# Kernel tuning notes

Hardware: AMD Instinct MI355X
Metric: run time of the kernel (lower is better)

## Reference

```python
import jax, jax.numpy as jnp
import numpy as np
import math

B, S, E, H = 2, 2048, 1024, 16
D = E // H  # head dim = 64


def setup_inputs() -> dict:
    key = jax.random.key(0)
    ks = jax.random.split(key, 7)
    scale = 1.0 / math.sqrt(E)
    return {
        "query": jax.random.normal(ks[0], (B, S, E), dtype=jnp.float32),
        "key": jax.random.normal(ks[1], (B, S, E), dtype=jnp.float32),
        "value": jax.random.normal(ks[2], (B, S, E), dtype=jnp.float32),
        # packed in-projection: (3E, E) weights, (3E,) bias, q/k/v order
        "in_proj_weight": jax.random.normal(ks[3], (3 * E, E), dtype=jnp.float32) * scale,
        "in_proj_bias": jnp.zeros((3 * E,), dtype=jnp.float32),
        "out_proj_weight": jax.random.normal(ks[4], (E, E), dtype=jnp.float32) * scale,
        "out_proj_bias": jnp.zeros((E,), dtype=jnp.float32),
    }


def reference(query, key, value, in_proj_weight, in_proj_bias, out_proj_weight, out_proj_bias):
    # packed in-projection (q, k, v order), F.linear convention: x @ W^T + b
    w_q, w_k, w_v = jnp.split(in_proj_weight, 3, axis=0)
    b_q, b_k, b_v = jnp.split(in_proj_bias, 3, axis=0)
    q = query @ w_q.T + b_q   # [B, S, E]
    k = key @ w_k.T + b_k
    v = value @ w_v.T + b_v

    # split heads: [B, S, E] -> [B, H, S, D]
    def heads(x):
        return x.reshape(B, S, H, D).transpose(0, 2, 1, 3)

    q, k, v = heads(q), heads(k), heads(v)
    q = q / jnp.asarray(math.sqrt(D), dtype=q.dtype)

    # naive softmax attention (materializes [B, H, S, S] as original bmm+softmax+bmm)
    scores = jnp.einsum("bhqd,bhkd->bhqk", q, k)
    attn = jax.nn.softmax(scores, axis=-1)
    out = jnp.einsum("bhqk,bhkd->bhqd", attn, v)  # [B, H, S, D]

    out = out.transpose(0, 2, 1, 3).reshape(B, S, E)
    return out @ out_proj_weight.T + out_proj_bias
```

## Files before the change

### kernel.cpp

```cpp
#include <hip/hip_runtime.h>
#include <stdint.h>

#define LOG2E 1.44269504088896340736f

typedef __bf16 bf16x8 __attribute__((ext_vector_type(8)));
typedef float f32x4 __attribute__((ext_vector_type(4)));
typedef float f32x16 __attribute__((ext_vector_type(16)));

static constexpr int Bb = 2, Ss = 2048, Ee = 1024, Hh = 16, Dd = 64;
static constexpr int BSE = Bb * Ss * Ee;

static constexpr size_t OFF_QB    = 0;
static constexpr size_t OFF_KB    = 4194304;
static constexpr size_t OFF_VB    = 8388608;
static constexpr size_t OFF_WQKV  = 12582912;
static constexpr size_t OFF_WOUT  = 15728640;
static constexpr size_t OFF_QH    = 16777216;
static constexpr size_t OFF_KH    = 20971520;
static constexpr size_t OFF_VH    = 25165824;
static constexpr size_t OFF_OB    = 29360128;

__device__ __forceinline__ uint16_t f32_bf16(float f) {
    uint32_t u = __builtin_bit_cast(uint32_t, f);
    u += 0x7fffu + ((u >> 16) & 1u);
    return (uint16_t)(u >> 16);
}

__device__ __forceinline__ uint32_t cvt_pk_bf16(float a, float b) {
    uint32_t r;
    asm("v_cvt_pk_bf16_f32 %0, %1, %2" : "=v"(r) : "v"(a), "v"(b));
    return r;
}

__device__ __forceinline__ void perm32swap(uint32_t& x, uint32_t& y) {
    asm("v_permlane32_swap_b32 %0, %1" : "+v"(x), "+v"(y));
}

__global__ __launch_bounds__(256) void cvt_kernel(
    const float* __restrict__ q, const float* __restrict__ k, const float* __restrict__ v,
    const float* __restrict__ w1, uint16_t* __restrict__ ws)
{
    const float* srcs[4] = {q, k, v, w1};
    const int ns4[4] = {BSE/4, BSE/4, BSE/4, (3*Ee*Ee)/4};
    uint16_t* dsts[4] = {ws+OFF_QB, ws+OFF_KB, ws+OFF_VB, ws+OFF_WQKV};
    int z = blockIdx.z;
    int i = blockIdx.x * blockDim.x + threadIdx.x;
    if (i < ns4[z]) {
        float4 f = ((const float4*)srcs[z])[i];
        ushort4 o;
        o.x = f32_bf16(f.x); o.y = f32_bf16(f.y);
        o.z = f32_bf16(f.z); o.w = f32_bf16(f.w);
        ((ushort4*)dsts[z])[i] = o;
    }
}

__global__ __launch_bounds__(256) void cvt_one(
    const float* __restrict__ src, uint16_t* __restrict__ dst)
{
    int i = blockIdx.x * 256 + threadIdx.x;
    float4 f = ((const float4*)src)[i];
    ushort4 o;
    o.x = f32_bf16(f.x); o.y = f32_bf16(f.y);
    o.z = f32_bf16(f.z); o.w = f32_bf16(f.w);
    ((ushort4*)dst)[i] = o;
}

template<int MODE>
__global__ __launch_bounds__(256) void gemm_nt(
    const uint16_t* __restrict__ Aq, const uint16_t* __restrict__ Ak,
    const uint16_t* __restrict__ Av, const uint16_t* __restrict__ Bw,
    const float* __restrict__ bias, uint16_t* __restrict__ OutB,
    float* __restrict__ OutF)
{
    constexpr int K = Ee, N = Ee;
    const int tid = threadIdx.x;
    const int l = tid & 63, w = tid >> 6;
    const int wr = w >> 1, wc = w & 1;
    const int z = (MODE == 0) ? blockIdx.z : 0;
    const int tm = 4 * blockIdx.x + (blockIdx.y >> 3);
    const int tn = blockIdx.y & 7;

    const uint16_t* A = (MODE == 0) ? (z == 0 ? Aq : (z == 1 ? Ak : Av)) : Aq;
    const uint16_t* Bp = Bw + (size_t)z * Ee * Ee;
    const float* bp = bias + (size_t)z * Ee;
    const size_t zoff = (size_t)(z == 2 ? 3 : z) * BSE;

    __shared__ alignas(16) uint16_t As[128 * 32];
    __shared__ alignas(16) uint16_t Bs[128 * 32];

    f32x4 acc[4][4] = {};
    const int arow = tm * 128;
    const int bcol = tn * 128;

    for (int kt = 0; kt < K / 32; ++kt) {
        __syncthreads();
        #pragma unroll
        for (int it = 0; it < 2; ++it) {
            int c = tid + it * 256;
            int row = c >> 2, qq = c & 3;
            const uint16_t* ga = A  + (size_t)(arow + row) * K + kt * 32 + qq * 8;
            const uint16_t* gb = Bp + (size_t)(bcol + row) * K + kt * 32 + qq * 8;
            __builtin_amdgcn_global_load_lds(
                (const __attribute__((address_space(1))) void*)ga,
                (__attribute__((address_space(3))) void*)(As + c * 8), 16, 0, 0);
            __builtin_amdgcn_global_load_lds(
                (const __attribute__((address_space(1))) void*)gb,
                (__attribute__((address_space(3))) void*)(Bs + c * 8), 16, 0, 0);
        }
        __syncthreads();
        bf16x8 aF[4], bF[4];
        #pragma unroll
        for (int m = 0; m < 4; ++m)
            aF[m] = *(const bf16x8*)(As + ((wr * 64 + m * 16 + (l & 15)) * 32 + (l >> 4) * 8));
        #pragma unroll
        for (int n = 0; n < 4; ++n)
            bF[n] = *(const bf16x8*)(Bs + ((wc * 64 + n * 16 + (l & 15)) * 32 + (l >> 4) * 8));
        #pragma unroll
        for (int m = 0; m < 4; ++m)
            #pragma unroll
            for (int n = 0; n < 4; ++n)
                acc[m][n] = __builtin_amdgcn_mfma_f32_16x16x32_bf16(aF[m], bF[n], acc[m][n], 0, 0, 0);
    }

    #pragma unroll
    for (int n = 0; n < 4; ++n) {
        int col = bcol + wc * 64 + n * 16 + (l & 15);
        float bn = bp[col];
        #pragma unroll
        for (int m = 0; m < 4; ++m) {
            int row0 = arow + wr * 64 + m * 16 + (l >> 4) * 4;
            #pragma unroll
            for (int j = 0; j < 4; ++j) {
                int row = row0 + j;
                float v = acc[m][n][j] + bn;
                if (MODE == 0) {
                    if (z == 0) v *= 0.125f * LOG2E;
                    int b = row >> 11, s = row & 2047, hh = col >> 6, d = col & 63;
                    OutB[zoff + (size_t)(((b * Hh) + hh) * Ss + s) * Dd + d] = f32_bf16(v);
                } else {
                    OutF[(size_t)row * N + col] = v;
                }
            }
        }
    }
}

__global__ __launch_bounds__(256) void vtr_kernel(
    const uint16_t* __restrict__ src, uint16_t* __restrict__ dst)
{
    __shared__ uint32_t T32[64][33];
    const int tid = threadIdx.x;
    const int bh = blockIdx.y;
    const int s0 = blockIdx.x * 64;
    const uint16_t* S = src + ((size_t)bh * Ss + s0) * Dd;
    {
        int rp = tid >> 3, d8 = tid & 7;
        uint4 a = *(const uint4*)(S + (size_t)(2 * rp) * Dd + d8 * 8);
        uint4 b = *(const uint4*)(S + (size_t)(2 * rp + 1) * Dd + d8 * 8);
        const uint16_t* ea = (const uint16_t*)&a;
        const uint16_t* eb = (const uint16_t*)&b;
        #pragma unroll
        for (int e = 0; e < 8; ++e)
            T32[d8 * 8 + e][rp] = (uint32_t)ea[e] | ((uint32_t)eb[e] << 16);
    }
    __syncthreads();
    uint16_t* Dp = dst + (size_t)bh * Dd * Ss + s0;
    {
        int d = tid >> 3, rpc = (tid & 7) * 4;
        #pragma unroll
        for (int half = 0; half < 2; ++half) {
            int dd = d + 32 * half;
            union { uint32_t u[4]; uint4 v; } pk;
            #pragma unroll
            for (int j = 0; j < 4; ++j) pk.u[j] = T32[dd][rpc + j];
            *(uint4*)(Dp + (size_t)dd * Ss + rpc * 2) = pk.v;
        }
    }
}

__global__ __launch_bounds__(256, 3) void attn_kernel(
    const uint16_t* __restrict__ Qh, const uint16_t* __restrict__ Kh,
    const uint16_t* __restrict__ Vtg, float* __restrict__ po,
    float* __restrict__ lpart)
{
    const int tid = threadIdx.x;
    const int l = tid & 63, w = tid >> 6;
    const int q = l & 31, hi = l >> 5;

    const int orig = blockIdx.x;
    const int L = (orig & 7) * 128 + (orig >> 3);
    const int qb = L & 15, split = (L >> 4) & 1, bh = L >> 5;

    const int q0 = qb * 128;
    const int keyb = split * 1024;
    const size_t baseK = (size_t)bh * Ss * Dd;
    const size_t baseV = (size_t)bh * Dd * Ss;

    __shared__ alignas(16) uint16_t Ks[2][64 * 64];
    __shared__ alignas(16) uint16_t Vt[2][64 * 64];

    bf16x8 qf[4];
    {
        const uint16_t* qp = Qh + baseK + (size_t)(q0 + w * 32 + q) * Dd + hi * 8;
        #pragma unroll
        for (int m = 0; m < 4; ++m) qf[m] = *(const bf16x8*)(qp + 16 * m);
    }

    auto stage = [&](int kt, int buf) {
        const int key0 = keyb + kt * 64;
        #pragma unroll
        for (int it = 0; it < 2; ++it) {
            int c = tid + 256 * it, row = c >> 3, cc = c & 7;
            const uint16_t* gk = Kh + baseK + (size_t)(key0 + row) * Dd + ((cc ^ (row & 7)) * 8);
            __builtin_amdgcn_global_load_lds(
                (const __attribute__((address_space(1))) void*)gk,
                (__attribute__((address_space(3))) void*)(&Ks[buf][c * 8]), 16, 0, 0);
        }
        #pragma unroll
        for (int it = 0; it < 2; ++it) {
            int c = tid + 256 * it, d = c >> 3, j = c & 7;
            const uint16_t* gv = Vtg + baseV + (size_t)d * Ss + key0 + 8 * (j ^ (d & 7) ^ (d >> 3));
            __builtin_amdgcn_global_load_lds(
                (const __attribute__((address_space(1))) void*)gv,
                (__attribute__((address_space(3))) void*)(&Vt[buf][c * 8]), 16, 0, 0);
        }
    };

    stage(0, 0);

    f32x16 o0 = {}, o1 = {};
    float lsum = 0.f;

    auto build_pb = [&](const f32x16& sv, bf16x8* pbout) {
        uint32_t W[4][2];
        #pragma unroll
        for (int a = 0; a < 4; ++a) {
            float p0 = __builtin_amdgcn_exp2f(sv[4 * a + 0]);
            float p1 = __builtin_amdgcn_exp2f(sv[4 * a + 1]);
            float p2 = __builtin_amdgcn_exp2f(sv[4 * a + 2]);
            float p3 = __builtin_amdgcn_exp2f(sv[4 * a + 3]);
            lsum += (p0 + p1) + (p2 + p3);
            W[a][0] = cvt_pk_bf16(p0, p1);
            W[a][1] = cvt_pk_bf16(p2, p3);
        }
        #pragma unroll
        for (int kl = 0; kl < 2; ++kl) {
            uint32_t x0 = W[2 * kl][0], x1 = W[2 * kl][1];
            uint32_t y0 = W[2 * kl + 1][0], y1 = W[2 * kl + 1][1];
            perm32swap(x0, y0);
            perm32swap(x1, y1);
            union { uint32_t u[4]; bf16x8 v; } pu;
            pu.u[0] = x0; pu.u[1] = x1; pu.u[2] = y0; pu.u[3] = y1;
            pbout[kl] = pu.v;
        }
    };

    #pragma unroll 2
    for (int kt = 0; kt < 16; ++kt) {
        const int b = kt & 1;
        __syncthreads();

        if (kt < 15) stage(kt + 1, b ^ 1);

        f32x16 s0 = {}, s1 = {};
        __builtin_amdgcn_s_setprio(1);
        #pragma unroll
        for (int m = 0; m < 4; ++m) {
            int sw = ((2 * m + hi) ^ (q & 7)) << 3;
            bf16x8 k0 = *(const bf16x8*)&Ks[b][q * 64 + sw];
            bf16x8 k1 = *(const bf16x8*)&Ks[b][(32 + q) * 64 + sw];
            s0 = __builtin_amdgcn_mfma_f32_32x32x16_bf16(k0, qf[m], s0, 0, 0, 0);
            s1 = __builtin_amdgcn_mfma_f32_32x32x16_bf16(k1, qf[m], s1, 0, 0, 0);
        }
        __builtin_amdgcn_s_setprio(0);

        bf16x8 pb[4];
        build_pb(s0, pb + 0);
        build_pb(s1, pb + 2);

        __builtin_amdgcn_s_setprio(1);
        #pragma unroll
        for (int ka = 0; ka < 4; ++ka) {
            #pragma unroll
            for (int dt = 0; dt < 2; ++dt) {
                int d = 32 * dt + q;
                int swz = (2 * ka + hi) ^ (d & 7) ^ (d >> 3);
                bf16x8 vf = *(const bf16x8*)&Vt[b][d * 64 + swz * 8];
                if (dt == 0)
                    o0 = __builtin_amdgcn_mfma_f32_32x32x16_bf16(vf, pb[ka], o0, 0, 0, 0);
                else
                    o1 = __builtin_amdgcn_mfma_f32_32x32x16_bf16(vf, pb[ka], o1, 0, 0, 0);
            }
        }
        __builtin_amdgcn_s_setprio(0);
    }

    float lr = lsum + __shfl_xor(lsum, 32);
    const int qrow = q0 + w * 32 + q;
    const int sb = split * 32 + bh;
    if (hi == 0) lpart[(size_t)sb * 2048 + qrow] = lr;
    #pragma unroll
    for (int dt = 0; dt < 2; ++dt) {
        const f32x16& oo = dt ? o1 : o0;
        #pragma unroll
        for (int rr = 0; rr < 16; ++rr) {
            int d = 32 * dt + (rr & 3) + 8 * (rr >> 2) + 4 * hi;
            po[((size_t)sb * 64 + d) * 2048 + qrow] = oo[rr];
        }
    }
}

__global__ __launch_bounds__(256) void combine_kernel(
    const float* __restrict__ po, const float* __restrict__ lp,
    uint16_t* __restrict__ Ob)
{
    __shared__ float T[64][65];
    const int t = threadIdx.x;
    const int bh = blockIdx.y;
    const int q0 = blockIdx.x * 64;
    const int qq = t & 63;
    const float inv = 1.0f / (lp[bh * 2048 + q0 + qq] + lp[(32 + bh) * 2048 + q0 + qq]);
    const size_t b0 = (size_t)bh * 64 * 2048;
    const size_t b1 = (size_t)(32 + bh) * 64 * 2048;
    #pragma unroll
    for (int i = 0; i < 16; ++i) {
        int d = i * 4 + (t >> 6);
        size_t off = (size_t)d * 2048 + q0 + qq;
        T[d][qq] = (po[b0 + off] + po[b1 + off]) * inv;
    }
    __syncthreads();
    const int row = t >> 2, dc = (t & 3) * 16;
    const int bb = bh >> 4, hh = bh & 15;
    union { uint16_t u[16]; uint4 v[2]; } pk;
    #pragma unroll
    for (int e = 0; e < 16; ++e) pk.u[e] = f32_bf16(T[dc + e][row]);
    uint16_t* dst = &Ob[(size_t)(bb * 2048 + q0 + row) * 1024 + hh * 64 + dc];
    *(uint4*)dst = pk.v[0];
    *((uint4*)dst + 1) = pk.v[1];
}

extern "C" void kernel_launch(void* const* d_in, const int* in_sizes, int n_in,
                              void* d_out, int out_size, void* d_ws, size_t ws_size,
                              hipStream_t stream) {
    (void)in_sizes; (void)n_in; (void)out_size; (void)ws_size;
    const float* query = (const float*)d_in[0];
    const float* key   = (const float*)d_in[1];
    const float* value = (const float*)d_in[2];
    const float* w_in  = (const float*)d_in[3];
    const float* b_in  = (const float*)d_in[4];
    const float* w_out = (const float*)d_in[5];
    const float* b_out = (const float*)d_in[6];
    uint16_t* ws = (uint16_t*)d_ws;

    uint16_t* qb    = ws + OFF_QB;
    uint16_t* kb    = ws + OFF_KB;
    uint16_t* vb    = ws + OFF_VB;
    uint16_t* wqkvb = ws + OFF_WQKV;
    uint16_t* woutb = ws + OFF_WOUT;
    uint16_t* Qh    = ws + OFF_QH;
    uint16_t* Kh    = ws + OFF_KH;
    uint16_t* Vtg   = ws + OFF_VH;
    uint16_t* Vsd   = ws + OFF_OB;
    uint16_t* Ob    = ws + OFF_OB;
    float*    po    = (float*)d_ws;
    float*    lpart = (float*)d_out;

    cvt_kernel<<<dim3(4096, 1, 4), 256, 0, stream>>>(query, key, value, w_in, ws);
    gemm_nt<0><<<dim3(8, 32, 3), 256, 0, stream>>>(qb, kb, vb, wqkvb, b_in, Qh, nullptr);
    vtr_kernel<<<dim3(32, 32), 256, 0, stream>>>(Vsd, Vtg);
    attn_kernel<<<dim3(1024), 256, 0, stream>>>(Qh, Kh, Vtg, po, lpart);
    combine_kernel<<<dim3(32, 32), 256, 0, stream>>>(po, lpart, Ob);
    cvt_one<<<dim3(1024), 256, 0, stream>>>(w_out, woutb);
    gemm_nt<1><<<dim3(8, 32, 1), 256, 0, stream>>>(Ob, nullptr, nullptr, woutb, b_out, nullptr, (float*)d_out);
}
```

Baseline: 137.0 us.

## Drop split-K attention and fuse normalization and bf16 output into attention kernel

The attention kernel now covers all 2048 keys per block (512 blocks instead of 1024 split blocks). It normalizes by the row sum and writes bf16 output through an LDS-swizzled transpose, so the combine kernel and its fp32 partial-output round trip go away. The out-projection weight conversion is folded into the main conversion launch, removing another kernel. The trade is half as many attention blocks with longer serial loops, plus a lower occupancy hint (2 instead of 3), which may hurt latency hiding and load balance across CUs.

New measurement: 127.7 us. -6.8%, faster.

```diff
diff --git a/kernel.cpp b/kernel.cpp
--- a/kernel.cpp
+++ b/kernel.cpp
@@ -38,11 +38,11 @@
 
 __global__ __launch_bounds__(256) void cvt_kernel(
     const float* __restrict__ q, const float* __restrict__ k, const float* __restrict__ v,
-    const float* __restrict__ w1, uint16_t* __restrict__ ws)
+    const float* __restrict__ w1, const float* __restrict__ w2, uint16_t* __restrict__ ws)
 {
-    const float* srcs[4] = {q, k, v, w1};
-    const int ns4[4] = {BSE/4, BSE/4, BSE/4, (3*Ee*Ee)/4};
-    uint16_t* dsts[4] = {ws+OFF_QB, ws+OFF_KB, ws+OFF_VB, ws+OFF_WQKV};
+    const float* srcs[5] = {q, k, v, w1, w2};
+    const int ns4[5] = {BSE/4, BSE/4, BSE/4, (3*Ee*Ee)/4, (Ee*Ee)/4};
+    uint16_t* dsts[5] = {ws+OFF_QB, ws+OFF_KB, ws+OFF_VB, ws+OFF_WQKV, ws+OFF_WOUT};
     int z = blockIdx.z;
     int i = blockIdx.x * blockDim.x + threadIdx.x;
     if (i < ns4[z]) {
@@ -52,17 +52,6 @@
         o.z = f32_bf16(f.z); o.w = f32_bf16(f.w);
         ((ushort4*)dsts[z])[i] = o;
     }
-}
-
-__global__ __launch_bounds__(256) void cvt_one(
-    const float* __restrict__ src, uint16_t* __restrict__ dst)
-{
-    int i = blockIdx.x * 256 + threadIdx.x;
-    float4 f = ((const float4*)src)[i];
-    ushort4 o;
-    o.x = f32_bf16(f.x); o.y = f32_bf16(f.y);
-    o.z = f32_bf16(f.z); o.w = f32_bf16(f.w);
-    ((ushort4*)dst)[i] = o;
 }
 
 template<int MODE>
@@ -178,21 +167,19 @@
     }
 }
 
-__global__ __launch_bounds__(256, 3) void attn_kernel(
+__global__ __launch_bounds__(256, 2) void attn_kernel(
     const uint16_t* __restrict__ Qh, const uint16_t* __restrict__ Kh,
-    const uint16_t* __restrict__ Vtg, float* __restrict__ po,
-    float* __restrict__ lpart)
+    const uint16_t* __restrict__ Vtg, uint16_t* __restrict__ Ob)
 {
     const int tid = threadIdx.x;
     const int l = tid & 63, w = tid >> 6;
     const int q = l & 31, hi = l >> 5;
 
     const int orig = blockIdx.x;
-    const int L = (orig & 7) * 128 + (orig >> 3);
-    const int qb = L & 15, split = (L >> 4) & 1, bh = L >> 5;
+    const int L = (orig & 7) * 64 + (orig >> 3);
+    const int qb = L & 15, bh = L >> 4;
 
     const int q0 = qb * 128;
-    const int keyb = split * 1024;
     const size_t baseK = (size_t)bh * Ss * Dd;
     const size_t baseV = (size_t)bh * Dd * Ss;
 
@@ -207,7 +194,7 @@
     }
 
     auto stage = [&](int kt, int buf) {
-        const int key0 = keyb + kt * 64;
+        const int key0 = kt * 64;
         #pragma unroll
         for (int it = 0; it < 2; ++it) {
             int c = tid + 256 * it, row = c >> 3, cc = c & 7;
@@ -256,11 +243,11 @@
     };
 
     #pragma unroll 2
-    for (int kt = 0; kt < 16; ++kt) {
+    for (int kt = 0; kt < 32; ++kt) {
         const int b = kt & 1;
         __syncthreads();
 
-        if (kt < 15) stage(kt + 1, b ^ 1);
+        if (kt < 31) stage(kt + 1, b ^ 1);
 
         f32x16 s0 = {}, s1 = {};
         __builtin_amdgcn_s_setprio(1);
@@ -296,47 +283,28 @@
     }
 
     float lr = lsum + __shfl_xor(lsum, 32);
-    const int qrow = q0 + w * 32 + q;
-    const int sb = split * 32 + bh;
-    if (hi == 0) lpart[(size_t)sb * 2048 + qrow] = lr;
+    const float inv = 1.0f / lr;
+    __syncthreads();
+    uint16_t* Os = &Ks[0][0];
+    const int ql = w * 32 + q;
     #pragma unroll
     for (int dt = 0; dt < 2; ++dt) {
         const f32x16& oo = dt ? o1 : o0;
         #pragma unroll
         for (int rr = 0; rr < 16; ++rr) {
             int d = 32 * dt + (rr & 3) + 8 * (rr >> 2) + 4 * hi;
-            po[((size_t)sb * 64 + d) * 2048 + qrow] = oo[rr];
-        }
-    }
-}
-
-__global__ __launch_bounds__(256) void combine_kernel(
-    const float* __restrict__ po, const float* __restrict__ lp,
-    uint16_t* __restrict__ Ob)
-{
-    __shared__ float T[64][65];
-    const int t = threadIdx.x;
-    const int bh = blockIdx.y;
-    const int q0 = blockIdx.x * 64;
-    const int qq = t & 63;
-    const float inv = 1.0f / (lp[bh * 2048 + q0 + qq] + lp[(32 + bh) * 2048 + q0 + qq]);
-    const size_t b0 = (size_t)bh * 64 * 2048;
-    const size_t b1 = (size_t)(32 + bh) * 64 * 2048;
+            Os[ql * 64 + (((d >> 3) ^ (ql & 7)) << 3) + (d & 7)] = f32_bf16(oo[rr] * inv);
+        }
+    }
+    __syncthreads();
+    const int bq = bh >> 4, hh = bh & 15;
     #pragma unroll
-    for (int i = 0; i < 16; ++i) {
-        int d = i * 4 + (t >> 6);
-        size_t off = (size_t)d * 2048 + q0 + qq;
-        T[d][qq] = (po[b0 + off] + po[b1 + off]) * inv;
-    }
-    __syncthreads();
-    const int row = t >> 2, dc = (t & 3) * 16;
-    const int bb = bh >> 4, hh = bh & 15;
-    union { uint16_t u[16]; uint4 v[2]; } pk;
-    #pragma unroll
-    for (int e = 0; e < 16; ++e) pk.u[e] = f32_bf16(T[dc + e][row]);
-    uint16_t* dst = &Ob[(size_t)(bb * 2048 + q0 + row) * 1024 + hh * 64 + dc];
-    *(uint4*)dst = pk.v[0];
-    *((uint4*)dst + 1) = pk.v[1];
+    for (int it = 0; it < 4; ++it) {
+        int qr = it * 32 + (tid >> 3);
+        int c = tid & 7;
+        bf16x8 vv = *(const bf16x8*)&Os[qr * 64 + ((c ^ (qr & 7)) << 3)];
+        *(bf16x8*)(Ob + (size_t)(bq * Ss + q0 + qr) * Ee + hh * Dd + c * 8) = vv;
+    }
 }
 
 extern "C" void kernel_launch(void* const* d_in, const int* in_sizes, int n_in,
@@ -362,14 +330,10 @@
     uint16_t* Vtg   = ws + OFF_VH;
     uint16_t* Vsd   = ws + OFF_OB;
     uint16_t* Ob    = ws + OFF_OB;
-    float*    po    = (float*)d_ws;
-    float*    lpart = (float*)d_out;
-
-    cvt_kernel<<<dim3(4096, 1, 4), 256, 0, stream>>>(query, key, value, w_in, ws);
+
+    cvt_kernel<<<dim3(4096, 1, 5), 256, 0, stream>>>(query, key, value, w_in, w_out, ws);
     gemm_nt<0><<<dim3(8, 32, 3), 256, 0, stream>>>(qb, kb, vb, wqkvb, b_in, Qh, nullptr);
     vtr_kernel<<<dim3(32, 32), 256, 0, stream>>>(Vsd, Vtg);
-    attn_kernel<<<dim3(1024), 256, 0, stream>>>(Qh, Kh, Vtg, po, lpart);
-    combine_kernel<<<dim3(32, 32), 256, 0, stream>>>(po, lpart, Ob);
-    cvt_one<<<dim3(1024), 256, 0, stream>>>(w_out, woutb);
+    attn_kernel<<<dim3(512), 256, 0, stream>>>(Qh, Kh, Vtg, Ob);
     gemm_nt<1><<<dim3(8, 32, 1), 256, 0, stream>>>(Ob, nullptr, nullptr, woutb, b_out, nullptr, (float*)d_out);
 }
```
